# Optimization experiments

Hardware: AMD Instinct MI355X
Metric: run time of the kernel (lower is better)

The kernel has to match this reference:

```python
import jax, jax.numpy as jnp
import numpy as np
from jax import lax

B, T, I, H, O = 64, 2048, 128, 256, 1


def setup_inputs() -> dict:
    key = jax.random.key(0)
    ks = jax.random.split(key, 8)
    lim_ih = 1.0 / np.sqrt(H)
    inp = {
        "xd": jax.random.normal(ks[0], (B, T, I), jnp.float32),
        "w": jax.random.normal(ks[1], (B, T, I), jnp.float32),
        # eqx.nn.LSTMCell params: gates stacked [i, f, g, o] along first axis
        "W_ih": jax.random.uniform(ks[2], (4 * H, I), jnp.float32, -lim_ih, lim_ih),
        "b_ih": jax.random.uniform(ks[3], (4 * H,), jnp.float32, -lim_ih, lim_ih),
        "W_hh": jax.random.uniform(ks[4], (4 * H, H), jnp.float32, -lim_ih, lim_ih),
        "b_hh": jax.random.uniform(ks[5], (4 * H,), jnp.float32, -lim_ih, lim_ih),
        "W_out": jax.random.uniform(ks[6], (O, H), jnp.float32, -lim_ih, lim_ih),
        "b_out": jax.random.uniform(ks[7], (O,), jnp.float32, -lim_ih, lim_ih),
    }
    return inp


def reference(xd, w, W_ih, b_ih, W_hh, b_hh, W_out, b_out):
    # Input gating (elementwise), then precompute the input-to-gates GEMM for
    # the whole sequence (mathematically identical to doing it per step).
    gated = xd * jax.nn.sigmoid(w)                       # [B,T,I]
    x_part = jnp.einsum("bti,gi->btg", gated, W_ih) + b_ih  # [B,T,4H]
    x_part = jnp.swapaxes(x_part, 0, 1)                  # [T,B,4H] for scan

    def step(state, xp):
        h, c = state
        z = xp + h @ W_hh.T + b_hh                       # [B,4H]
        i, f, g, o = jnp.split(z, 4, axis=-1)            # eqx gate order i,f,g,o
        c = jax.nn.sigmoid(f) * c + jax.nn.sigmoid(i) * jnp.tanh(g)
        h = jax.nn.sigmoid(o) * jnp.tanh(c)
        return (h, c), None

    init = (jnp.zeros((B, H), xd.dtype), jnp.zeros((B, H), xd.dtype))
    (h_T, _), _ = lax.scan(step, init, x_part)
    return h_T @ W_out.T + b_out                         # [B,O]
```

## Files before the change

kernel.cpp:

```cpp
#include <hip/hip_runtime.h>
#include <hip/hip_fp16.h>
#include <stdint.h>


#define NB 64
#define NT 2048
#define NI 128
#define NH 256

typedef _Float16 h8_t __attribute__((ext_vector_type(8)));
typedef _Float16 h4_t __attribute__((ext_vector_type(4)));
typedef float f4_t __attribute__((ext_vector_type(4)));

__device__ __forceinline__ float sigm(float x) {
  return __builtin_amdgcn_rcpf(1.f + __expf(-x));
}
__device__ __forceinline__ float tanh_f(float x) {
  return 1.f - 2.f * __builtin_amdgcn_rcpf(1.f + __expf(2.f * x));
}


__launch_bounds__(256, 1)
__global__ void lstm_persist(
    const float* __restrict__ xd, const float* __restrict__ w,
    const float* __restrict__ W_ih, const float* __restrict__ b_ih,
    const float* __restrict__ W_hh, const float* __restrict__ b_hh,
    const float* __restrict__ W_out, const float* __restrict__ b_out,
    float* __restrict__ out, uint64_t* ex)
{
  const int bid = blockIdx.x;
  const int g = bid & 7;
  const int p = bid >> 3;
  const int tid = threadIdx.x;
  const int lane = tid & 63;
  const int wv = tid >> 6;

  __shared__ _Float16 Alds[16][392];
  __shared__ float Zlds[128][17];

  for (int i = tid; i < 16 * 392; i += 256) (&Alds[0][0])[i] = (_Float16)0.f;

  const int q  = lane >> 4;
  const int cc = lane & 15;

  h8_t wf[2][12];
  for (int nt = 0; nt < 2; ++nt) {
    int r = 16 * (2 * wv + nt) + cc;
    int R = (r & 3) * NH + p * 32 + (r >> 2);
    for (int kt = 0; kt < 12; ++kt) {
      int k = kt * 32 + q * 8;
      const float* s = (k < NI) ? (W_ih + (size_t)R * NI + k)
                                : (W_hh + (size_t)R * NH + (k - NI));
      f4_t lo = *(const f4_t*)s;
      f4_t hi = *(const f4_t*)(s + 4);
      h8_t hh;
      hh[0] = (_Float16)lo[0]; hh[1] = (_Float16)lo[1];
      hh[2] = (_Float16)lo[2]; hh[3] = (_Float16)lo[3];
      hh[4] = (_Float16)hi[0]; hh[5] = (_Float16)hi[1];
      hh[6] = (_Float16)hi[2]; hh[7] = (_Float16)hi[3];
      wf[nt][kt] = hh;
    }
  }

  const int bl = tid >> 5;
  const int jj = tid & 31;
  float bias[4];
  #pragma unroll
  for (int gate = 0; gate < 4; ++gate)
    bias[gate] = b_ih[gate * NH + p * 32 + jj] + b_hh[gate * NH + p * 32 + jj];

  int pidx[7];
  #pragma unroll
  for (int s7 = 0; s7 < 7; ++s7) {
    int ps = (s7 < p) ? s7 : s7 + 1;
    pidx[s7] = g * 2048 + ps * 256 + bl * 32 + jj;
  }
  uint64_t* const myslot0 = ex + g * 2048 + p * 256 + bl * 32 + jj;

  float creg = 0.f;
  float hreg = 0.f;
  const size_t xbase = ((size_t)(g * 8 + bl) * NT) * NI + jj * 4;

  __syncthreads();

  for (int t = 0; t < NT; ++t) {
    f4_t xv = *(const f4_t*)(xd + xbase + (size_t)t * NI);
    f4_t wg = *(const f4_t*)(w  + xbase + (size_t)t * NI);

    if (t > 0) {
      const uint64_t* base = ex + (t & 1) * 16384;
      unsigned need = 0x7f;
      uint64_t v[7];
      while (need) {
        #pragma unroll
        for (int s7 = 0; s7 < 7; ++s7)
          if (need & (1u << s7))
            v[s7] = __hip_atomic_load(base + pidx[s7], __ATOMIC_RELAXED,
                                      __HIP_MEMORY_SCOPE_AGENT);
        #pragma unroll
        for (int s7 = 0; s7 < 7; ++s7)
          if ((need & (1u << s7)) && (unsigned)(v[s7] >> 32) == (unsigned)t) {
            int ps = (s7 < p) ? s7 : s7 + 1;
            Alds[bl][NI + ps * 32 + jj] =
                (_Float16)__uint_as_float((unsigned)v[s7]);
            need &= ~(1u << s7);
          }
      }
    }

    h4_t gx;
    gx[0] = (_Float16)(xv[0] * sigm(wg[0]));
    gx[1] = (_Float16)(xv[1] * sigm(wg[1]));
    gx[2] = (_Float16)(xv[2] * sigm(wg[2]));
    gx[3] = (_Float16)(xv[3] * sigm(wg[3]));
    *(h4_t*)(&Alds[bl][jj * 4]) = gx;
    __syncthreads();

    f4_t acc0 = {0.f, 0.f, 0.f, 0.f}, acc1 = {0.f, 0.f, 0.f, 0.f};
    #pragma unroll
    for (int kt = 0; kt < 12; ++kt) {
      h8_t af = *(const h8_t*)(&Alds[cc][kt * 32 + q * 8]);
      acc0 = __builtin_amdgcn_mfma_f32_16x16x32_f16(af, wf[0][kt], acc0, 0, 0, 0);
      acc1 = __builtin_amdgcn_mfma_f32_16x16x32_f16(af, wf[1][kt], acc1, 0, 0, 0);
    }
    if (q < 2) {
      #pragma unroll
      for (int r = 0; r < 4; ++r) {
        Zlds[16 * (2 * wv)     + cc][q * 4 + r] = acc0[r];
        Zlds[16 * (2 * wv + 1) + cc][q * 4 + r] = acc1[r];
      }
    }
    __syncthreads();

    float zi = Zlds[jj * 4 + 0][bl] + bias[0];
    float zf = Zlds[jj * 4 + 1][bl] + bias[1];
    float zg = Zlds[jj * 4 + 2][bl] + bias[2];
    float zo = Zlds[jj * 4 + 3][bl] + bias[3];
    creg = sigm(zf) * creg + sigm(zi) * tanh_f(zg);
    hreg = sigm(zo) * tanh_f(creg);
    Alds[bl][NI + p * 32 + jj] = (_Float16)hreg;
    uint64_t pay = ((uint64_t)(unsigned)(t + 1) << 32) | __float_as_uint(hreg);
    __hip_atomic_store(myslot0 + ((t + 1) & 1) * 16384, pay,
                       __ATOMIC_RELAXED, __HIP_MEMORY_SCOPE_AGENT);
  }

  if (p == 0) {
    float sum = hreg * W_out[jj];
    unsigned need = 0x7f;
    uint64_t v[7];
    float hv[7];
    while (need) {
      #pragma unroll
      for (int s7 = 0; s7 < 7; ++s7)
        if (need & (1u << s7))
          v[s7] = __hip_atomic_load(ex + pidx[s7], __ATOMIC_RELAXED,
                                    __HIP_MEMORY_SCOPE_AGENT);
      #pragma unroll
      for (int s7 = 0; s7 < 7; ++s7)
        if ((need & (1u << s7)) && (unsigned)(v[s7] >> 32) == (unsigned)NT) {
          hv[s7] = __uint_as_float((unsigned)v[s7]);
          need &= ~(1u << s7);
        }
    }
    #pragma unroll
    for (int s7 = 0; s7 < 7; ++s7) {
      int ps = (s7 < p) ? s7 : s7 + 1;
      sum += hv[s7] * W_out[ps * 32 + jj];
    }
    #pragma unroll
    for (int m = 16; m >= 1; m >>= 1) sum += __shfl_xor(sum, m, 64);
    if (jj == 0) out[g * 8 + bl] = sum + b_out[0];
  }
}

extern "C" void kernel_launch(void* const* d_in, const int* in_sizes, int n_in,
                              void* d_out, int out_size, void* d_ws, size_t ws_size,
                              hipStream_t stream) {
  (void)in_sizes; (void)n_in; (void)out_size; (void)ws_size;
  const float* xd    = (const float*)d_in[0];
  const float* w     = (const float*)d_in[1];
  const float* W_ih  = (const float*)d_in[2];
  const float* b_ih  = (const float*)d_in[3];
  const float* W_hh  = (const float*)d_in[4];
  const float* b_hh  = (const float*)d_in[5];
  const float* W_out = (const float*)d_in[6];
  const float* b_out = (const float*)d_in[7];
  uint64_t* ex = (uint64_t*)d_ws;
  lstm_persist<<<dim3(64), dim3(256), 0, stream>>>(
      xd, w, W_ih, b_ih, W_hh, b_hh, W_out, b_out, (float*)d_out, ex);
}
```

Before: 4.353 ms.

## Repartition persistent LSTM into 16 blocks with overlapped h exchange

Changes the partition from 8 batch groups by 8 hidden slices (64 blocks) to 4 batch groups of 16 rows by 4 hidden slices of 64 units (16 blocks). Each wave now holds 4 MFMA column tiles and each block exchanges h with only 3 peers. The h values travel as packed fp16 pairs, so each flag word carries two values. The input-gate part of the GEMM (first 4 k-tiles) runs before waiting on peer h, and the next step's x/w loads are prefetched, hiding the cross-block latency. This cuts synchronisation fan-in and parallelises per step across fewer CUs. The cost is more register pressure (48 h8 weight fragments) and more serial MFMA work per block.

Result: slower. 6.226 ms (+43.0%).

```diff
diff --git a/kernel.cpp b/kernel.cpp
--- a/kernel.cpp
+++ b/kernel.cpp
@@ -3,10 +3,14 @@
 #include <stdint.h>
 
 
-#define NB 64
 #define NT 2048
 #define NI 128
 #define NH 256
+#define NG 4
+#define NP 4
+#define BG 16
+#define JS 64
+#define HBUF 8192
 
 typedef _Float16 h8_t __attribute__((ext_vector_type(8)));
 typedef _Float16 h4_t __attribute__((ext_vector_type(4)));
@@ -17,6 +21,13 @@
 }
 __device__ __forceinline__ float tanh_f(float x) {
   return 1.f - 2.f * __builtin_amdgcn_rcpf(1.f + __expf(2.f * x));
+}
+__device__ __forceinline__ uint32_t f16b(float x) {
+  _Float16 h = (_Float16)x;
+  return (uint32_t)__builtin_bit_cast(uint16_t, h);
+}
+__device__ __forceinline__ _Float16 b2h(uint32_t u) {
+  return __builtin_bit_cast(_Float16, (uint16_t)(u & 0xffffu));
 }
 
 
@@ -29,24 +40,25 @@
     float* __restrict__ out, uint64_t* ex)
 {
   const int bid = blockIdx.x;
-  const int g = bid & 7;
-  const int p = bid >> 3;
+  const int g = bid >> 2;
+  const int p = bid & 3;
   const int tid = threadIdx.x;
   const int lane = tid & 63;
   const int wv = tid >> 6;
-
-  __shared__ _Float16 Alds[16][392];
-  __shared__ float Zlds[128][17];
-
-  for (int i = tid; i < 16 * 392; i += 256) (&Alds[0][0])[i] = (_Float16)0.f;
-
   const int q  = lane >> 4;
   const int cc = lane & 15;
-
-  h8_t wf[2][12];
-  for (int nt = 0; nt < 2; ++nt) {
-    int r = 16 * (2 * wv + nt) + cc;
-    int R = (r & 3) * NH + p * 32 + (r >> 2);
+  const int b   = tid >> 4;
+  const int jl2 = tid & 15;
+
+  __shared__ _Float16 Alds[16][392];
+  __shared__ float Zlds[16][260];
+
+  for (int i = tid; i < 16 * 392; i += 256) (&Alds[0][0])[i] = (_Float16)0.f;
+
+  h8_t wf[4][12];
+  for (int ntl = 0; ntl < 4; ++ntl) {
+    int r = 16 * (wv * 4 + ntl) + cc;
+    int R = (r & 3) * NH + p * JS + (r >> 2);
     for (int kt = 0; kt < 12; ++kt) {
       int k = kt * 32 + q * 8;
       const float* s = (k < NI) ? (W_ih + (size_t)R * NI + k)
@@ -58,118 +70,170 @@
       hh[2] = (_Float16)lo[2]; hh[3] = (_Float16)lo[3];
       hh[4] = (_Float16)hi[0]; hh[5] = (_Float16)hi[1];
       hh[6] = (_Float16)hi[2]; hh[7] = (_Float16)hi[3];
-      wf[nt][kt] = hh;
-    }
-  }
-
-  const int bl = tid >> 5;
-  const int jj = tid & 31;
-  float bias[4];
+      wf[ntl][kt] = hh;
+    }
+  }
+
+  float bias[4][4];
   #pragma unroll
-  for (int gate = 0; gate < 4; ++gate)
-    bias[gate] = b_ih[gate * NH + p * 32 + jj] + b_hh[gate * NH + p * 32 + jj];
-
-  int pidx[7];
+  for (int i = 0; i < 4; ++i) {
+    int jg = p * JS + jl2 * 4 + i;
+    #pragma unroll
+    for (int gate = 0; gate < 4; ++gate)
+      bias[i][gate] = b_ih[gate * NH + jg] + b_hh[gate * NH + jg];
+  }
+
+  int pp[3]; { int c = 0; for (int i = 0; i < 4; ++i) if (i != p) pp[c++] = i; }
+  int psl[3];
   #pragma unroll
-  for (int s7 = 0; s7 < 7; ++s7) {
-    int ps = (s7 < p) ? s7 : s7 + 1;
-    pidx[s7] = g * 2048 + ps * 256 + bl * 32 + jj;
-  }
-  uint64_t* const myslot0 = ex + g * 2048 + p * 256 + bl * 32 + jj;
-
-  float creg = 0.f;
-  float hreg = 0.f;
-  const size_t xbase = ((size_t)(g * 8 + bl) * NT) * NI + jj * 4;
+  for (int s = 0; s < 3; ++s)
+    psl[s] = (((g * 4 + pp[s]) * 16 + b) * 16 + jl2) * 2;
+  const int myslot = (((g * 4 + p) * 16 + b) * 16 + jl2) * 2;
+
+  float cst[4] = {0.f, 0.f, 0.f, 0.f};
+  float hval[4] = {0.f, 0.f, 0.f, 0.f};
+
+  const size_t xrow = ((size_t)(g * BG + b) * NT) * NI + jl2 * 8;
+  f4_t xa = *(const f4_t*)(xd + xrow);
+  f4_t xb = *(const f4_t*)(xd + xrow + 4);
+  f4_t wa = *(const f4_t*)(w + xrow);
+  f4_t wb = *(const f4_t*)(w + xrow + 4);
 
   __syncthreads();
 
   for (int t = 0; t < NT; ++t) {
-    f4_t xv = *(const f4_t*)(xd + xbase + (size_t)t * NI);
-    f4_t wg = *(const f4_t*)(w  + xbase + (size_t)t * NI);
-
+    uint64_t pv[6];
+    const uint64_t* hb = ex + (t & 1) * HBUF;
     if (t > 0) {
-      const uint64_t* base = ex + (t & 1) * 16384;
-      unsigned need = 0x7f;
-      uint64_t v[7];
+      #pragma unroll
+      for (int s = 0; s < 3; ++s) {
+        pv[2 * s]     = __hip_atomic_load(hb + psl[s], __ATOMIC_RELAXED,
+                                          __HIP_MEMORY_SCOPE_AGENT);
+        pv[2 * s + 1] = __hip_atomic_load(hb + psl[s] + 1, __ATOMIC_RELAXED,
+                                          __HIP_MEMORY_SCOPE_AGENT);
+      }
+    }
+
+    h8_t gx;
+    gx[0] = (_Float16)(xa[0] * sigm(wa[0]));
+    gx[1] = (_Float16)(xa[1] * sigm(wa[1]));
+    gx[2] = (_Float16)(xa[2] * sigm(wa[2]));
+    gx[3] = (_Float16)(xa[3] * sigm(wa[3]));
+    gx[4] = (_Float16)(xb[0] * sigm(wb[0]));
+    gx[5] = (_Float16)(xb[1] * sigm(wb[1]));
+    gx[6] = (_Float16)(xb[2] * sigm(wb[2]));
+    gx[7] = (_Float16)(xb[3] * sigm(wb[3]));
+    *(h8_t*)(&Alds[b][jl2 * 8]) = gx;
+    {
+      size_t xo = xrow + (size_t)((t + 1 < NT) ? t + 1 : NT - 1) * NI;
+      xa = *(const f4_t*)(xd + xo);
+      xb = *(const f4_t*)(xd + xo + 4);
+      wa = *(const f4_t*)(w + xo);
+      wb = *(const f4_t*)(w + xo + 4);
+    }
+    __syncthreads();
+
+    f4_t acc[4];
+    #pragma unroll
+    for (int n = 0; n < 4; ++n) acc[n] = (f4_t){0.f, 0.f, 0.f, 0.f};
+    #pragma unroll
+    for (int kt = 0; kt < 4; ++kt) {
+      h8_t af = *(const h8_t*)(&Alds[cc][kt * 32 + q * 8]);
+      #pragma unroll
+      for (int n = 0; n < 4; ++n)
+        acc[n] = __builtin_amdgcn_mfma_f32_16x16x32_f16(af, wf[n][kt], acc[n], 0, 0, 0);
+    }
+
+    if (t > 0) {
+      unsigned need = 0x7;
       while (need) {
         #pragma unroll
-        for (int s7 = 0; s7 < 7; ++s7)
-          if (need & (1u << s7))
-            v[s7] = __hip_atomic_load(base + pidx[s7], __ATOMIC_RELAXED,
-                                      __HIP_MEMORY_SCOPE_AGENT);
-        #pragma unroll
-        for (int s7 = 0; s7 < 7; ++s7)
-          if ((need & (1u << s7)) && (unsigned)(v[s7] >> 32) == (unsigned)t) {
-            int ps = (s7 < p) ? s7 : s7 + 1;
-            Alds[bl][NI + ps * 32 + jj] =
-                (_Float16)__uint_as_float((unsigned)v[s7]);
-            need &= ~(1u << s7);
+        for (int s = 0; s < 3; ++s) {
+          if (!(need & (1u << s))) continue;
+          unsigned t0 = (unsigned)(pv[2 * s] >> 32);
+          unsigned t1 = (unsigned)(pv[2 * s + 1] >> 32);
+          if (t0 == (unsigned)t && t1 == (unsigned)t) {
+            uint32_t a0 = (uint32_t)pv[2 * s];
+            uint32_t a1 = (uint32_t)pv[2 * s + 1];
+            h4_t hp;
+            hp[0] = b2h(a0); hp[1] = b2h(a0 >> 16);
+            hp[2] = b2h(a1); hp[3] = b2h(a1 >> 16);
+            *(h4_t*)(&Alds[b][NI + pp[s] * JS + jl2 * 4]) = hp;
+            need &= ~(1u << s);
+          } else {
+            pv[2 * s]     = __hip_atomic_load(hb + psl[s], __ATOMIC_RELAXED,
+                                              __HIP_MEMORY_SCOPE_AGENT);
+            pv[2 * s + 1] = __hip_atomic_load(hb + psl[s] + 1, __ATOMIC_RELAXED,
+                                              __HIP_MEMORY_SCOPE_AGENT);
           }
+        }
       }
     }
-
-    h4_t gx;
-    gx[0] = (_Float16)(xv[0] * sigm(wg[0]));
-    gx[1] = (_Float16)(xv[1] * sigm(wg[1]));
-    gx[2] = (_Float16)(xv[2] * sigm(wg[2]));
-    gx[3] = (_Float16)(xv[3] * sigm(wg[3]));
-    *(h4_t*)(&Alds[bl][jj * 4]) = gx;
     __syncthreads();
 
-    f4_t acc0 = {0.f, 0.f, 0.f, 0.f}, acc1 = {0.f, 0.f, 0.f, 0.f};
-    #pragma unroll
-    for (int kt = 0; kt < 12; ++kt) {
+    #pragma unroll
+    for (int kt = 4; kt < 12; ++kt) {
       h8_t af = *(const h8_t*)(&Alds[cc][kt * 32 + q * 8]);
-      acc0 = __builtin_amdgcn_mfma_f32_16x16x32_f16(af, wf[0][kt], acc0, 0, 0, 0);
-      acc1 = __builtin_amdgcn_mfma_f32_16x16x32_f16(af, wf[1][kt], acc1, 0, 0, 0);
-    }
-    if (q < 2) {
-      #pragma unroll
-      for (int r = 0; r < 4; ++r) {
-        Zlds[16 * (2 * wv)     + cc][q * 4 + r] = acc0[r];
-        Zlds[16 * (2 * wv + 1) + cc][q * 4 + r] = acc1[r];
+      #pragma unroll
+      for (int n = 0; n < 4; ++n)
+        acc[n] = __builtin_amdgcn_mfma_f32_16x16x32_f16(af, wf[n][kt], acc[n], 0, 0, 0);
+    }
+    #pragma unroll
+    for (int n = 0; n < 4; ++n) {
+      int zr = 16 * (wv * 4 + n) + cc;
+      #pragma unroll
+      for (int rr = 0; rr < 4; ++rr)
+        Zlds[q * 4 + rr][zr] = acc[n][rr];
+    }
+    __syncthreads();
+
+    h4_t hh;
+    #pragma unroll
+    for (int i = 0; i < 4; ++i) {
+      f4_t zz = *(const f4_t*)(&Zlds[b][(jl2 * 4 + i) * 4]);
+      float zi = zz[0] + bias[i][0];
+      float zf = zz[1] + bias[i][1];
+      float zg = zz[2] + bias[i][2];
+      float zo = zz[3] + bias[i][3];
+      cst[i] = sigm(zf) * cst[i] + sigm(zi) * tanh_f(zg);
+      hval[i] = sigm(zo) * tanh_f(cst[i]);
+      hh[i] = (_Float16)hval[i];
+    }
+    *(h4_t*)(&Alds[b][NI + p * JS + jl2 * 4]) = hh;
+    uint64_t tagw = ((uint64_t)(unsigned)(t + 1)) << 32;
+    uint64_t w0 = tagw | (f16b(hval[0]) | (f16b(hval[1]) << 16));
+    uint64_t w1 = tagw | (f16b(hval[2]) | (f16b(hval[3]) << 16));
+    uint64_t* ob = ex + ((t + 1) & 1) * HBUF + myslot;
+    __hip_atomic_store(ob, w0, __ATOMIC_RELAXED, __HIP_MEMORY_SCOPE_AGENT);
+    __hip_atomic_store(ob + 1, w1, __ATOMIC_RELAXED, __HIP_MEMORY_SCOPE_AGENT);
+  }
+
+  f4_t wo = *(const f4_t*)(W_out + p * JS + jl2 * 4);
+  float ps = hval[0] * wo[0] + hval[1] * wo[1] + hval[2] * wo[2] + hval[3] * wo[3];
+  #pragma unroll
+  for (int m = 1; m < 16; m <<= 1) ps += __shfl_xor(ps, m, 64);
+  uint64_t* ex2 = ex + 2 * HBUF;
+  if (jl2 == 0) {
+    uint64_t pw = (((uint64_t)2049u) << 32) | (uint64_t)__float_as_uint(ps);
+    __hip_atomic_store(ex2 + (g * 4 + p) * 16 + b, pw,
+                       __ATOMIC_RELAXED, __HIP_MEMORY_SCOPE_AGENT);
+  }
+  if (p == 0 && tid < 16) {
+    float sum = b_out[0];
+    unsigned need = 0xF;
+    while (need) {
+      #pragma unroll
+      for (int pq = 0; pq < 4; ++pq) {
+        if (!(need & (1u << pq))) continue;
+        uint64_t v = __hip_atomic_load(ex2 + (g * 4 + pq) * 16 + tid,
+                                       __ATOMIC_RELAXED, __HIP_MEMORY_SCOPE_AGENT);
+        if ((unsigned)(v >> 32) == 2049u) {
+          sum += __uint_as_float((unsigned)v);
+          need &= ~(1u << pq);
+        }
       }
     }
-    __syncthreads();
-
-    float zi = Zlds[jj * 4 + 0][bl] + bias[0];
-    float zf = Zlds[jj * 4 + 1][bl] + bias[1];
-    float zg = Zlds[jj * 4 + 2][bl] + bias[2];
-    float zo = Zlds[jj * 4 + 3][bl] + bias[3];
-    creg = sigm(zf) * creg + sigm(zi) * tanh_f(zg);
-    hreg = sigm(zo) * tanh_f(creg);
-    Alds[bl][NI + p * 32 + jj] = (_Float16)hreg;
-    uint64_t pay = ((uint64_t)(unsigned)(t + 1) << 32) | __float_as_uint(hreg);
-    __hip_atomic_store(myslot0 + ((t + 1) & 1) * 16384, pay,
-                       __ATOMIC_RELAXED, __HIP_MEMORY_SCOPE_AGENT);
-  }
-
-  if (p == 0) {
-    float sum = hreg * W_out[jj];
-    unsigned need = 0x7f;
-    uint64_t v[7];
-    float hv[7];
-    while (need) {
-      #pragma unroll
-      for (int s7 = 0; s7 < 7; ++s7)
-        if (need & (1u << s7))
-          v[s7] = __hip_atomic_load(ex + pidx[s7], __ATOMIC_RELAXED,
-                                    __HIP_MEMORY_SCOPE_AGENT);
-      #pragma unroll
-      for (int s7 = 0; s7 < 7; ++s7)
-        if ((need & (1u << s7)) && (unsigned)(v[s7] >> 32) == (unsigned)NT) {
-          hv[s7] = __uint_as_float((unsigned)v[s7]);
-          need &= ~(1u << s7);
-        }
-    }
-    #pragma unroll
-    for (int s7 = 0; s7 < 7; ++s7) {
-      int ps = (s7 < p) ? s7 : s7 + 1;
-      sum += hv[s7] * W_out[ps * 32 + jj];
-    }
-    #pragma unroll
-    for (int m = 16; m >= 1; m >>= 1) sum += __shfl_xor(sum, m, 64);
-    if (jj == 0) out[g * 8 + bl] = sum + b_out[0];
+    out[g * BG + tid] = sum;
   }
 }
 
@@ -186,6 +250,6 @@
   const float* W_out = (const float*)d_in[6];
   const float* b_out = (const float*)d_in[7];
   uint64_t* ex = (uint64_t*)d_ws;
-  lstm_persist<<<dim3(64), dim3(256), 0, stream>>>(
+  lstm_persist<<<dim3(16), dim3(256), 0, stream>>>(
       xd, w, W_ih, b_ih, W_hh, b_hh, W_out, b_out, (float*)d_out, ex);
 }
```
